# Kernel tuning notes

Hardware: AMD Instinct MI355X
Metric: run time of the kernel (lower is better)

The kernel has to match this reference:

```python
import jax, jax.numpy as jnp
import numpy as np

NUM_CLASSES = 2
TOP_K = 1500
CONF_THRESH = 0.01
NMS_THRESH = 0.2
VAR0, VAR1 = 0.1, 0.2  # cfg['variance']


def setup_inputs() -> dict:
    key = jax.random.key(0)
    k1, k2, k3 = jax.random.split(key, 3)
    B, P = 32, 76800
    loc_data = jax.random.normal(k1, (B, P, 4), jnp.float32)
    conf_data = jax.random.uniform(k2, (B * P, NUM_CLASSES), jnp.float32)
    prior_data = jax.random.uniform(k3, (P, 4), jnp.float32)
    return {"loc_data": loc_data, "conf_data": conf_data, "prior_data": prior_data}


def _decode(loc, priors):
    # loc, priors: [P,4]; SSD box decode with variances
    cxcy = priors[:, :2] + loc[:, :2] * VAR0 * priors[:, 2:]
    wh = priors[:, 2:] * jnp.exp(loc[:, 2:] * VAR1)
    x1y1 = cxcy - wh * 0.5
    return jnp.concatenate([x1y1, x1y1 + wh], axis=-1)  # [P,4] (x1,y1,x2,y2)


def _nms_per_class(scores, boxes):
    # scores: [P], boxes: [P,4] -> [TOP_K,5] packed (score,x1,y1,x2,y2)
    s = jnp.where(scores > CONF_THRESH, scores, -jnp.inf)
    sk, idx = jax.lax.top_k(s, TOP_K)  # torch nms keeps only top_k candidates
    bk = boxes[idx]
    x1, y1, x2, y2 = bk[:, 0], bk[:, 1], bk[:, 2], bk[:, 3]
    area = (x2 - x1) * (y2 - y1)
    iota = jnp.arange(TOP_K)

    def step(active, i):
        # greedy NMS over score-descending candidates
        xx1 = jnp.maximum(x1, x1[i]); yy1 = jnp.maximum(y1, y1[i])
        xx2 = jnp.minimum(x2, x2[i]); yy2 = jnp.minimum(y2, y2[i])
        inter = jnp.maximum(xx2 - xx1, 0.0) * jnp.maximum(yy2 - yy1, 0.0)
        iou = inter / (area + area[i] - inter)
        kept = active[i]
        suppress = (iou > NMS_THRESH) & (iota != i)
        active = jnp.where(kept, active & ~suppress, active)
        return active, kept

    _, keep = jax.lax.scan(step, sk > -jnp.inf, iota)
    rows = jnp.where(keep[:, None], jnp.concatenate([sk[:, None], bk], axis=1), 0.0)
    # pack kept rows at the front (score-descending order), zeros after
    rank = jnp.cumsum(keep) - 1
    dest = jnp.where(keep, rank, TOP_K)  # dump non-kept into scratch slot
    return jnp.zeros((TOP_K + 1, 5), bk.dtype).at[dest].set(rows)[:TOP_K]


def reference(loc_data, conf_data, prior_data):
    B, P, _ = loc_data.shape
    conf = conf_data.reshape(B, P, NUM_CLASSES)
    decoded = jax.vmap(_decode, in_axes=(0, None))(loc_data, prior_data)  # [B,P,4]
    outs = []
    for cl in range(1, NUM_CLASSES):  # background class 0 stays zero
        outs.append(jax.vmap(_nms_per_class)(conf[:, :, cl], decoded))
    bg = jnp.zeros((B, 1, TOP_K, 5), decoded.dtype)
    return jnp.concatenate([bg, jnp.stack(outs, axis=1)], axis=1)  # [B,C,TOP_K,5]
```

## Files before the change

kernel.cpp:

```cpp
#include <hip/hip_runtime.h>
#include <stdint.h>

typedef unsigned long long u64;
typedef unsigned int u32;

#define NUM_B 32
#define NUM_P 76800
#define TOPK 1500
#define NBINS 2048
#define CAP 2048
#define NWORDS 24
#define NCHUNK 6
#define HSLICES 16
#define HCHUNK (NUM_P / HSLICES)

__device__ __forceinline__ u32 fbits(float f) { return __float_as_uint(f); }
__device__ __forceinline__ int binOf(float s) {
    int b = (int)(s * (float)NBINS);
    return (b > NBINS - 1) ? NBINS - 1 : b;
}
__device__ __forceinline__ u64 readlane64(u64 v, int l) {
    u32 lo = (u32)__builtin_amdgcn_readlane((int)(u32)(v & 0xffffffffu), l);
    u32 hi = (u32)__builtin_amdgcn_readlane((int)(u32)(v >> 32), l);
    return ((u64)hi << 32) | lo;
}

__global__ __launch_bounds__(256) void hist_kernel(const float4* __restrict__ conf4,
                                                   u32* __restrict__ hist,
                                                   u32* __restrict__ bpos) {
    int c = blockIdx.x, b = blockIdx.y, tid = threadIdx.x;
    if (tid < NBINS / HSLICES) bpos[(size_t)b * NBINS + c * (NBINS / HSLICES) + tid] = 0;
    __shared__ u32 h[NBINS];
    for (int i = tid; i < NBINS; i += 256) h[i] = 0;
    __syncthreads();
    const float4* base = conf4 + (size_t)b * (NUM_P / 2) + (size_t)c * (HCHUNK / 2);
    for (int i = tid; i < HCHUNK / 2; i += 256) {
        float4 v = base[i];
        if (v.y > 0.01f) atomicAdd(&h[binOf(v.y)], 1u);
        if (v.w > 0.01f) atomicAdd(&h[binOf(v.w)], 1u);
    }
    __syncthreads();
    u32* outp = hist + ((size_t)b * HSLICES + c) * NBINS;
    for (int i = tid; i < NBINS; i += 256) outp[i] = h[i];
}

__global__ void thresh_kernel(const u32* __restrict__ hist, int* __restrict__ tbin,
                              u32* __restrict__ binbase, u32* __restrict__ bincnt,
                              u32* __restrict__ ntotal) {
    int b = blockIdx.x;
    int tid = threadIdx.x;
    const u32* hb = hist + (size_t)b * HSLICES * NBINS;
    __shared__ u32 vals[256];
    __shared__ int s_min;
    u32 total = 0;
    for (int c = 0; c < NBINS / 256; ++c) {
        if (tid == 0) s_min = 256;
        int bin = NBINS - 1 - (c * 256 + tid);
        u32 v = 0;
#pragma unroll
        for (int s = 0; s < HSLICES; ++s) v += hb[(size_t)s * NBINS + bin];
        __syncthreads();
        vals[tid] = v;
        __syncthreads();
        for (int off = 1; off < 256; off <<= 1) {
            u32 add = (tid >= off) ? vals[tid - off] : 0;
            __syncthreads();
            vals[tid] += add;
            __syncthreads();
        }
        u32 cum = total + vals[tid];
        binbase[(size_t)b * NBINS + bin] = cum - v;
        bincnt [(size_t)b * NBINS + bin] = v;
        if (cum >= TOPK) atomicMin(&s_min, tid);
        __syncthreads();
        if (s_min < 256) {
            if (tid == 0) {
                tbin[b] = NBINS - 1 - (c * 256 + s_min);
                ntotal[b] = total + vals[s_min];
            }
            return;
        }
        total += vals[255];
    }
    if (tid == 0) { tbin[b] = 0; ntotal[b] = total; }
}

__global__ __launch_bounds__(256) void compact_kernel(
    const float4* __restrict__ conf4, const int* __restrict__ tbin,
    const u32* __restrict__ binbase, u32* __restrict__ bpos,
    u64* __restrict__ keys) {
    int b = blockIdx.y;
    int tid = threadIdx.x;
    int f4 = blockIdx.x * 256 + tid;
    float4 c = conf4[(size_t)b * (NUM_P / 2) + f4];
    int tb = tbin[b];
    int p0 = f4 * 2, p1 = p0 + 1;

    int b0 = binOf(c.y);
    if (c.y > 0.01f && b0 >= tb) {
        u32 slot = atomicAdd(&bpos[(size_t)b * NBINS + b0], 1u);
        u32 pos = binbase[(size_t)b * NBINS + b0] + slot;
        if (pos < CAP) keys[(size_t)b * CAP + pos] = ((u64)fbits(c.y) << 32) | (u32)(~p0);
    }
    int b1 = binOf(c.w);
    if (c.w > 0.01f && b1 >= tb) {
        u32 slot = atomicAdd(&bpos[(size_t)b * NBINS + b1], 1u);
        u32 pos = binbase[(size_t)b * NBINS + b1] + slot;
        if (pos < CAP) keys[(size_t)b * CAP + pos] = ((u64)fbits(c.w) << 32) | (u32)(~p1);
    }
}

__global__ __launch_bounds__(256) void rank_decode_kernel(
    const u64* __restrict__ keys, const u32* __restrict__ binbase,
    const u32* __restrict__ bincnt, const u32* __restrict__ ntotal,
    const float* __restrict__ loc, const float* __restrict__ prior,
    float* __restrict__ sscore, float* __restrict__ sbox) {
#pragma clang fp contract(off)
    int b = blockIdx.y;
    int g = blockIdx.x * 256 + threadIdx.x;
    int n = (int)min(ntotal[b], (u32)CAP);
    if (g >= n) return;
    const u64* kb = keys + (size_t)b * CAP;
    u64 mykey = kb[g];
    float sc = __uint_as_float((u32)(mykey >> 32));
    int bn = binOf(sc);
    u32 start = binbase[(size_t)b * NBINS + bn];
    u32 end = start + bincnt[(size_t)b * NBINS + bn];
    if (end > (u32)n) end = (u32)n;
    u32 rank = start;
#pragma unroll 4
    for (u32 j = start; j < end; ++j) rank += (kb[j] > mykey) ? 1u : 0u;

    if (rank < TOPK) {
        u32 pidx = ~(u32)mykey;
        const float* lp = &loc[((size_t)b * NUM_P + pidx) * 4];
        const float* pp = &prior[(size_t)pidx * 4];
        float lx = lp[0], ly = lp[1], lw = lp[2], lh = lp[3];
        float pcx = pp[0], pcy = pp[1], pw = pp[2], ph = pp[3];
        float cx = pcx + (lx * 0.1f) * pw;
        float cy = pcy + (ly * 0.1f) * ph;
        float w  = pw * expf(lw * 0.2f);
        float h  = ph * expf(lh * 0.2f);
        float x1 = cx - w * 0.5f;
        float y1 = cy - h * 0.5f;
        float x2 = x1 + w;
        float y2 = y1 + h;
        sscore[(size_t)b * TOPK + rank] = sc;
        float* bx = &sbox[((size_t)b * TOPK + rank) * 4];
        bx[0] = x1; bx[1] = y1; bx[2] = x2; bx[3] = y2;
    }
}

__global__ __launch_bounds__(256) void mask_kernel(
    const float* __restrict__ sbox, u64* __restrict__ mask) {
#pragma clang fp contract(off)
    int w = blockIdx.x, c = blockIdx.y, b = blockIdx.z, tid = threadIdx.x;
    int i = c * 256 + tid;
    if ((w * 64 + 63) <= (c * 256)) return;
    __shared__ float4 cbox[64];
    __shared__ float car[64];
    if (tid < 64) {
        int j = w * 64 + tid;
        float4 bx = make_float4(0.f, 0.f, 0.f, 0.f);
        if (j < TOPK) bx = ((const float4*)sbox)[(size_t)b * TOPK + j];
        cbox[tid] = bx;
        car[tid] = (bx.z - bx.x) * (bx.w - bx.y);
    }
    __syncthreads();
    if (i < TOPK && (w * 64 + 63) > i) {
        const double MID = 0.5 * ((double)__uint_as_float(0x3E4CCCCDu) +
                                  (double)__uint_as_float(0x3E4CCCCEu));
        const float4 bx = ((const float4*)sbox)[(size_t)b * TOPK + i];
        float x1i = bx.x, y1i = bx.y, x2i = bx.z, y2i = bx.w;
        float ai = (x2i - x1i) * (y2i - y1i);
        u64 jmask = (i < w * 64) ? ~0ULL : (~0ULL << (i - w * 64 + 1));
        u64 m = 0;
        for (int j2 = 0; j2 < 64; ++j2) {
            float4 cb = cbox[j2];
            float xx1 = fmaxf(cb.x, x1i);
            float yy1 = fmaxf(cb.y, y1i);
            float xx2 = fminf(cb.z, x2i);
            float yy2 = fminf(cb.w, y2i);
            float iw = fmaxf(xx2 - xx1, 0.0f);
            float ih = fmaxf(yy2 - yy1, 0.0f);
            float inter = iw * ih;
            float denom = (car[j2] + ai) - inter;
            if ((double)inter >= MID * (double)denom) m |= (1ULL << j2);
        }
        m &= jmask;
        mask[((size_t)b * NWORDS + w) * TOPK + i] = m;
    }
}

__global__ __launch_bounds__(256) void sweep_kernel(
    const u64* __restrict__ mask, const float* __restrict__ sscore,
    const float* __restrict__ sbox, float* __restrict__ out) {
    int b = blockIdx.x, tid = threadIdx.x;
    int lane = tid & 63, wid = tid >> 6;

    const u64* mbase = mask + (size_t)b * NWORDS * TOPK;

    __shared__ u64 rowbuf[3][NWORDS][65];
    __shared__ u64 aw[NWORDS];
    __shared__ u32 pfx[NWORDS + 1];

    u64 act = 0;
    u64 sv[8];
    if (wid == 0) {
        for (int c = 0; c < NWORDS; ++c) {
            int r = c * 64 + lane;
            bool v = (r < TOPK) && (sscore[(size_t)b * TOPK + r] > 0.0f);
            u64 m = __ballot(v);
            if (lane == c) act = m;
        }
    } else {
        int w0 = (wid - 1) * 8;
#pragma unroll
        for (int t = 0; t < 2; ++t) {
            u64 tmp[8];
#pragma unroll
            for (int k = 0; k < 8; ++k)
                tmp[k] = (w0 + k >= t) ? mbase[(size_t)(w0 + k) * TOPK + t * 64 + lane] : 0ULL;
#pragma unroll
            for (int k = 0; k < 8; ++k)
                rowbuf[t][w0 + k][lane] = tmp[k];
        }
        {
            int rr = 2 * 64 + lane;
#pragma unroll
            for (int k = 0; k < 8; ++k)
                sv[k] = (w0 + k >= 2) ? mbase[(size_t)(w0 + k) * TOPK + rr] : 0ULL;
        }
    }
    __syncthreads();

    for (int T = 0; T < NWORDS; ++T) {
        if (wid == 0) {
            u64 dreg = rowbuf[T % 3][T][lane];
            u64 actw = readlane64(act, T);
            u64 kept = 0, rem = actw;
            while (rem) {
                int i2 = __ffsll(rem) - 1;
                kept |= (1ULL << i2);
                rem &= rem - 1;
                rem &= ~readlane64(dreg, i2);
            }
            if (lane == T) act = kept;
            if (lane > T && lane < NWORDS) {
                u64 kb = kept;
                while (kb) {
                    int r = __ffsll(kb) - 1;
                    kb &= kb - 1;
                    act &= ~rowbuf[T % 3][lane][r];
                }
            }
        } else {
            int tw = T + 2;
            if (tw < NWORDS) {
                int w0 = (wid - 1) * 8;
#pragma unroll
                for (int k = 0; k < 8; ++k)
                    rowbuf[tw % 3][w0 + k][lane] = sv[k];
                int tn = T + 3;
                if (tn < NWORDS) {
                    int rr = tn * 64 + lane;
                    bool vr = rr < TOPK;
#pragma unroll
                    for (int k = 0; k < 8; ++k)
                        sv[k] = (vr && (w0 + k >= tn))
                                    ? mbase[(size_t)(w0 + k) * TOPK + rr] : 0ULL;
                }
            }
        }
        __syncthreads();
    }

    if (wid == 0 && lane < NWORDS) aw[lane] = act;
    {
        float4* pz = (float4*)(out + (size_t)b * 2 * TOPK * 5);
        float4 z4 = make_float4(0.f, 0.f, 0.f, 0.f);
        for (int t = tid; t < (2 * TOPK * 5) / 4; t += 256) pz[t] = z4;
    }
    __syncthreads();
    if (tid == 0) {
        u32 acc = 0;
        for (int wd = 0; wd < NWORDS; ++wd) { pfx[wd] = acc; acc += (u32)__popcll(aw[wd]); }
        pfx[NWORDS] = acc;
    }
    __syncthreads();
    for (int r = tid; r < TOPK; r += 256) {
        int wd = r >> 6;
        u64 word = aw[wd];
        if ((word >> (r & 63)) & 1ULL) {
            u32 rank = pfx[wd] + (u32)__popcll(word & ((1ULL << (r & 63)) - 1ULL));
            float sc = sscore[(size_t)b * TOPK + r];
            float4 bx = ((const float4*)sbox)[(size_t)b * TOPK + r];
            size_t base_o = (((size_t)b * 2 + 1) * TOPK + (size_t)rank) * 5;
            out[base_o + 0] = sc;
            out[base_o + 1] = bx.x;
            out[base_o + 2] = bx.y;
            out[base_o + 3] = bx.z;
            out[base_o + 4] = bx.w;
        }
    }
}

extern "C" void kernel_launch(void* const* d_in, const int* in_sizes, int n_in,
                              void* d_out, int out_size, void* d_ws, size_t ws_size,
                              hipStream_t stream) {
    const float* loc   = (const float*)d_in[0];
    const float* conf  = (const float*)d_in[1];
    const float* prior = (const float*)d_in[2];
    float* out = (float*)d_out;
    char* ws = (char*)d_ws;

    u64* mask_buf = (u64*)(ws + 0);
    u32* hist     = (u32*)(ws + 0);
    u32* binbase  = (u32*)(ws + 4194304);
    u32* bincnt   = (u32*)(ws + 4456448);
    u32* bpos     = (u32*)(ws + 4718592);
    u64* keys     = (u64*)(ws + 4980736);
    int* tbin     = (int*)(ws + 5505024);
    u32* ntotal   = (u32*)(ws + 5505152);
    float* sscore = (float*)(ws + 9216000);
    float* sbox   = (float*)(ws + 9408000);

    hist_kernel<<<dim3(HSLICES, 32), 256, 0, stream>>>((const float4*)conf, hist, bpos);
    thresh_kernel<<<32, 256, 0, stream>>>(hist, tbin, binbase, bincnt, ntotal);
    compact_kernel<<<dim3(150, 32), 256, 0, stream>>>((const float4*)conf, tbin, binbase,
                                                      bpos, keys);
    rank_decode_kernel<<<dim3(CAP / 256, 32), 256, 0, stream>>>(keys, binbase, bincnt,
                                                                ntotal, loc, prior,
                                                                sscore, sbox);
    mask_kernel<<<dim3(NWORDS, NCHUNK, 32), 256, 0, stream>>>(sbox, mask_buf);
    sweep_kernel<<<32, 256, 0, stream>>>(mask_buf, sscore, sbox, out);
}
```

Baseline: 178.5 us.

## Preload all off-diagonal mask tiles into LDS and remove per-step block barriers in NMS sweep

The sweep kernel used to stream mask rows through a triple-buffered LDS ring, with a block-wide barrier on each of 24 steps. Now all 276 off-diagonal 64x64 tiles are loaded into shared memory up front, the diagonal tiles are held in registers of wave 0, and the greedy sweep runs in a single wave with no barriers. Suppression accumulation uses branchless masked ORs over 16-bit groups, and the other waves zero the output while the sweep runs. The cost is a large LDS footprint (about 143KB) and more register pressure for wave 0. The histogram kernel's threshold write is also simplified.

Result: slower. 195.2 us (+9.4%).

```diff
diff --git a/kernel.cpp b/kernel.cpp
--- a/kernel.cpp
+++ b/kernel.cpp
@@ -13,6 +13,7 @@
 #define NCHUNK 6
 #define HSLICES 16
 #define HCHUNK (NUM_P / HSLICES)
+#define NPAIR 276
 
 __device__ __forceinline__ u32 fbits(float f) { return __float_as_uint(f); }
 __device__ __forceinline__ int binOf(float s) {
@@ -74,10 +75,7 @@
         if (cum >= TOPK) atomicMin(&s_min, tid);
         __syncthreads();
         if (s_min < 256) {
-            if (tid == 0) {
-                tbin[b] = NBINS - 1 - (c * 256 + s_min);
-                ntotal[b] = total + vals[s_min];
-            }
+            if (tid == s_min) { tbin[b] = bin; ntotal[b] = cum; }
             return;
         }
         total += vals[255];
@@ -200,43 +198,64 @@
 
     const u64* mbase = mask + (size_t)b * NWORDS * TOPK;
 
-    __shared__ u64 rowbuf[3][NWORDS][65];
+    __shared__ u64 tb[NPAIR * 65];
     __shared__ u64 aw[NWORDS];
     __shared__ u32 pfx[NWORDS + 1];
 
     u64 act = 0;
-    u64 sv[8];
+    u64 dr[NWORDS];
+
     if (wid == 0) {
+#pragma unroll
+        for (int t = 0; t < NWORDS; ++t)
+            dr[t] = mbase[(size_t)t * TOPK + t * 64 + lane];
+        float sv[NWORDS];
+#pragma unroll
         for (int c = 0; c < NWORDS; ++c) {
             int r = c * 64 + lane;
-            bool v = (r < TOPK) && (sscore[(size_t)b * TOPK + r] > 0.0f);
-            u64 m = __ballot(v);
+            sv[c] = (r < TOPK) ? sscore[(size_t)b * TOPK + r] : 0.0f;
+        }
+#pragma unroll
+        for (int c = 0; c < NWORDS; ++c) {
+            u64 m = __ballot(sv[c] > 0.0f);
             if (lane == c) act = m;
         }
     } else {
-        int w0 = (wid - 1) * 8;
-#pragma unroll
-        for (int t = 0; t < 2; ++t) {
-            u64 tmp[8];
-#pragma unroll
-            for (int k = 0; k < 8; ++k)
-                tmp[k] = (w0 + k >= t) ? mbase[(size_t)(w0 + k) * TOPK + t * 64 + lane] : 0ULL;
-#pragma unroll
-            for (int k = 0; k < 8; ++k)
-                rowbuf[t][w0 + k][lane] = tmp[k];
+        int p0 = (wid - 1) * 92;
+        int t = 0, rm = p0;
+        while (rm >= NWORDS - 1 - t) { rm -= NWORDS - 1 - t; ++t; }
+        int w = t + 1 + rm;
+        int pbase = p0;
+        for (int ch = 0; ch < 11; ++ch) {
+            u64 tmp[8]; int lo[8];
+#pragma unroll
+            for (int k = 0; k < 8; ++k) {
+                tmp[k] = mbase[(size_t)w * TOPK + t * 64 + lane];
+                lo[k] = (pbase + k) * 65 + lane;
+                if (++w == NWORDS) { ++t; w = t + 1; }
+            }
+#pragma unroll
+            for (int k = 0; k < 8; ++k) tb[lo[k]] = tmp[k];
+            pbase += 8;
         }
         {
-            int rr = 2 * 64 + lane;
-#pragma unroll
-            for (int k = 0; k < 8; ++k)
-                sv[k] = (w0 + k >= 2) ? mbase[(size_t)(w0 + k) * TOPK + rr] : 0ULL;
-        }
-    }
-    __syncthreads();
-
-    for (int T = 0; T < NWORDS; ++T) {
-        if (wid == 0) {
-            u64 dreg = rowbuf[T % 3][T][lane];
+            u64 tmp[4]; int lo[4];
+#pragma unroll
+            for (int k = 0; k < 4; ++k) {
+                tmp[k] = mbase[(size_t)w * TOPK + t * 64 + lane];
+                lo[k] = (pbase + k) * 65 + lane;
+                if (++w == NWORDS) { ++t; w = t + 1; }
+            }
+#pragma unroll
+            for (int k = 0; k < 4; ++k) tb[lo[k]] = tmp[k];
+        }
+    }
+    __syncthreads();
+
+    if (wid == 0) {
+#pragma unroll
+        for (int T = 0; T < NWORDS; ++T) {
+            u64 dreg = dr[T];
             u64 actw = readlane64(act, T);
             u64 kept = 0, rem = actw;
             while (rem) {
@@ -247,39 +266,27 @@
             }
             if (lane == T) act = kept;
             if (lane > T && lane < NWORDS) {
-                u64 kb = kept;
-                while (kb) {
-                    int r = __ffsll(kb) - 1;
-                    kb &= kb - 1;
-                    act &= ~rowbuf[T % 3][lane][r];
+                const u64* rb = &tb[((T * (47 - T)) / 2 + (lane - T - 1)) * 65];
+                u64 acc = 0;
+#pragma unroll
+                for (int b16 = 0; b16 < 4; ++b16) {
+                    if ((u32)(kept >> (b16 * 16)) & 0xffffu) {
+#pragma unroll
+                        for (int j = 0; j < 16; ++j) {
+                            int r = b16 * 16 + j;
+                            u64 sel = (u64)0 - ((kept >> r) & 1ULL);
+                            acc |= rb[r] & sel;
+                        }
+                    }
                 }
+                act &= ~acc;
             }
-        } else {
-            int tw = T + 2;
-            if (tw < NWORDS) {
-                int w0 = (wid - 1) * 8;
-#pragma unroll
-                for (int k = 0; k < 8; ++k)
-                    rowbuf[tw % 3][w0 + k][lane] = sv[k];
-                int tn = T + 3;
-                if (tn < NWORDS) {
-                    int rr = tn * 64 + lane;
-                    bool vr = rr < TOPK;
-#pragma unroll
-                    for (int k = 0; k < 8; ++k)
-                        sv[k] = (vr && (w0 + k >= tn))
-                                    ? mbase[(size_t)(w0 + k) * TOPK + rr] : 0ULL;
-                }
-            }
-        }
-        __syncthreads();
-    }
-
-    if (wid == 0 && lane < NWORDS) aw[lane] = act;
-    {
+        }
+        if (lane < NWORDS) aw[lane] = act;
+    } else {
         float4* pz = (float4*)(out + (size_t)b * 2 * TOPK * 5);
         float4 z4 = make_float4(0.f, 0.f, 0.f, 0.f);
-        for (int t = tid; t < (2 * TOPK * 5) / 4; t += 256) pz[t] = z4;
+        for (int t2 = tid - 64; t2 < (2 * TOPK * 5) / 4; t2 += 192) pz[t2] = z4;
     }
     __syncthreads();
     if (tid == 0) {
```
